# Kernel optimization log

Measured on AMD Instinct MI355X. Metric: run time of the kernel, lower is better.

## Reference

```python
import jax, jax.numpy as jnp
import numpy as np

B, N, F_IN = 1, 4096, 128
H, F_OUT = 8, 64
NEG = -1e9


def setup_inputs() -> dict:
    key = jax.random.key(0)
    ks = jax.random.split(key, 7)
    x = jax.random.normal(ks[0], (B, N, F_IN), dtype=jnp.float32)
    edge = jax.random.uniform(ks[1], (N, N)) < 0.02
    edge = edge | jnp.eye(N, dtype=bool)
    adj = jnp.where(edge, 0.0, NEG).astype(jnp.float32)
    # Glorot-uniform params
    def glorot(k, shape, fan_in, fan_out):
        lim = float(np.sqrt(6.0 / (fan_in + fan_out)))
        return jax.random.uniform(k, shape, jnp.float32, -lim, lim)
    W_proj = glorot(ks[2], (H * F_OUT, F_IN), F_IN, H * F_OUT)      # linear_proj.weight
    a_src = glorot(ks[3], (1, H, F_OUT), H, F_OUT)                   # scoring_fn_source
    a_tgt = glorot(ks[4], (1, H, F_OUT), H, F_OUT)                   # scoring_fn_target
    W_skip = glorot(ks[5], (H * F_OUT, F_IN), F_IN, H * F_OUT)       # skip_proj.weight
    bias = jnp.zeros((H * F_OUT,), dtype=jnp.float32)
    return {"in_nodes_features": x, "adj": adj, "W_proj": W_proj,
            "a_src": a_src, "a_tgt": a_tgt, "W_skip": W_skip, "bias": bias}


def reference(in_nodes_features, adj, W_proj, a_src, a_tgt, W_skip, bias):
    x = in_nodes_features                                  # [B,N,Fin]  (dropout p=0)
    proj = jnp.einsum('bnf,of->bno', x, W_proj)            # [B,N,H*Fo]
    proj = proj.reshape(B, N, H, F_OUT)                    # [B,N,H,Fo]
    s_src = jnp.einsum('bnhd,xhd->bhn', proj, a_src)       # [B,H,N] (row / source)
    s_tgt = jnp.einsum('bnhd,xhd->bhn', proj, a_tgt)       # [B,H,N] (col / target)
    scores = s_src[:, :, :, None] + s_tgt[:, :, None, :]   # [B,H,N,N]
    scores = jax.nn.leaky_relu(scores, negative_slope=0.2)
    att = jax.nn.softmax(scores + adj, axis=-1)            # adj additive mask, broadcast over B,H
    out = jnp.einsum('bhij,bjhd->bihd', att, proj)         # [B,N,H,Fo]
    out = out + jnp.einsum('bnf,of->bno', x, W_skip).reshape(B, N, H, F_OUT)  # skip (dims differ)
    out = out.reshape(B, N, H * F_OUT) + bias              # concat + bias
    out = jax.nn.elu(out)                                  # activation ELU
    return out, adj
```

## Files before the change

### kernel.cpp

```cpp
#include <hip/hip_runtime.h>
#include <cmath>

#define N_NODES 4096
#define FIN     128
#define H_HEADS 8
#define FOUT    64
#define HF      512
#define CAP     256

typedef float  vf4 __attribute__((ext_vector_type(4)));
typedef float  vf2 __attribute__((ext_vector_type(2)));
typedef unsigned int vu4 __attribute__((ext_vector_type(4)));

__device__ __forceinline__ unsigned short f2bf(float f) {
    unsigned u = __float_as_uint(f);
    u += 0x7fff + ((u >> 16) & 1);
    return (unsigned short)(u >> 16);
}

__global__ __launch_bounds__(256) void gemm_fused(
    const float* __restrict__ x, const float* __restrict__ Wp,
    const float* __restrict__ Ws, const float* __restrict__ a_src,
    const float* __restrict__ a_tgt,
    unsigned short* __restrict__ proj, float* __restrict__ skip,
    float* __restrict__ ssrc, float* __restrict__ stgt)
{
    __shared__ __align__(16) float AsT[64][68];
    __shared__ __align__(16) float BsT[64][68];

    const int t  = threadIdx.x;
    const int rb = blockIdx.y * 64;
    const int cb = blockIdx.x * 64;
    const bool isP = (cb < HF);
    const float* Wbase = isP ? (Wp + cb * FIN) : (Ws + (cb - HF) * FIN);

    const int tx = t & 15;
    const int ty = t >> 4;
    float acc[4][4] = {{0.f}};

    for (int kb = 0; kb < FIN; kb += 64) {
        #pragma unroll
        for (int p = 0; p < 4; ++p) {
            int f4 = t + p * 256;
            int r  = f4 >> 4;
            int k4 = f4 & 15;
            float4 a = *(const float4*)(x + (size_t)(rb + r) * FIN + kb + k4 * 4);
            AsT[k4*4+0][r] = a.x; AsT[k4*4+1][r] = a.y;
            AsT[k4*4+2][r] = a.z; AsT[k4*4+3][r] = a.w;
            float4 b = *(const float4*)(Wbase + (size_t)r * FIN + kb + k4 * 4);
            BsT[k4*4+0][r] = b.x; BsT[k4*4+1][r] = b.y;
            BsT[k4*4+2][r] = b.z; BsT[k4*4+3][r] = b.w;
        }
        __syncthreads();
        #pragma unroll 8
        for (int kk = 0; kk < 64; ++kk) {
            float4 a = *(const float4*)&AsT[kk][ty * 4];
            float4 b = *(const float4*)&BsT[kk][tx * 4];
            acc[0][0] += a.x*b.x; acc[0][1] += a.x*b.y; acc[0][2] += a.x*b.z; acc[0][3] += a.x*b.w;
            acc[1][0] += a.y*b.x; acc[1][1] += a.y*b.y; acc[1][2] += a.y*b.z; acc[1][3] += a.y*b.w;
            acc[2][0] += a.z*b.x; acc[2][1] += a.z*b.y; acc[2][2] += a.z*b.z; acc[2][3] += a.z*b.w;
            acc[3][0] += a.w*b.x; acc[3][1] += a.w*b.y; acc[3][2] += a.w*b.z; acc[3][3] += a.w*b.w;
        }
        __syncthreads();
    }

    if (isP) {
        #pragma unroll
        for (int i = 0; i < 4; ++i) {
            ushort4 v;
            v.x = f2bf(acc[i][0]); v.y = f2bf(acc[i][1]);
            v.z = f2bf(acc[i][2]); v.w = f2bf(acc[i][3]);
            *(ushort4*)(proj + (size_t)(rb + ty*4 + i) * HF + cb + tx * 4) = v;
        }
        const int h = cb >> 6;
        const float as0 = a_src[cb + tx*4 + 0], as1 = a_src[cb + tx*4 + 1];
        const float as2 = a_src[cb + tx*4 + 2], as3 = a_src[cb + tx*4 + 3];
        const float at0 = a_tgt[cb + tx*4 + 0], at1 = a_tgt[cb + tx*4 + 1];
        const float at2 = a_tgt[cb + tx*4 + 2], at3 = a_tgt[cb + tx*4 + 3];
        #pragma unroll
        for (int i = 0; i < 4; ++i) {
            float ps = acc[i][0]*as0 + acc[i][1]*as1 + acc[i][2]*as2 + acc[i][3]*as3;
            float pt = acc[i][0]*at0 + acc[i][1]*at1 + acc[i][2]*at2 + acc[i][3]*at3;
            #pragma unroll
            for (int off = 1; off < 16; off <<= 1) {
                ps += __shfl_xor(ps, off);
                pt += __shfl_xor(pt, off);
            }
            if (tx == 0) {
                int n = rb + ty*4 + i;
                ssrc[n * H_HEADS + h] = ps;
                stgt[n * H_HEADS + h] = pt;
            }
        }
    } else {
        #pragma unroll
        for (int i = 0; i < 4; ++i) {
            float4 v = make_float4(acc[i][0], acc[i][1], acc[i][2], acc[i][3]);
            *(float4*)(skip + (size_t)(rb + ty*4 + i) * HF + (cb - HF) + tx * 4) = v;
        }
    }
}

__global__ __launch_bounds__(512) void att_kernel(
    const float* __restrict__ adj, const unsigned short* __restrict__ proj,
    const float* __restrict__ skip, const float* __restrict__ ssrc,
    const float* __restrict__ stgt, const float* __restrict__ bias,
    float* __restrict__ out, float* __restrict__ adj_out)
{
    __shared__ int   s_idx[CAP];
    __shared__ float sp[H_HEADS][CAP];
    __shared__ float s_i[H_HEADS];
    __shared__ int   s_cnt;

    const int t    = threadIdx.x;
    const int i    = blockIdx.x;
    const int lane = t & 63;
    if (t == 0) s_cnt = 0;
    if (t < H_HEADS) s_i[t] = ssrc[i * H_HEADS + t];
    __syncthreads();

    const vf4* arow = (const vf4*)(adj + (size_t)i * N_NODES);
    vf4 va[2];
    const unsigned long long lt = (1ull << lane) - 1ull;
    #pragma unroll
    for (int it = 0; it < 2; ++it) {
        const int f4 = t + it * 512;
        vf4 v = __builtin_nontemporal_load(arow + f4);
        va[it] = v;
        const int jb = (f4 * 4) << 10;
        const bool h0 = (v.x == 0.f), h1 = (v.y == 0.f), h2 = (v.z == 0.f), h3 = (v.w == 0.f);
        const unsigned long long b0 = __ballot(h0), b1 = __ballot(h1);
        const unsigned long long b2 = __ballot(h2), b3 = __ballot(h3);
        const int n0 = __popcll(b0), n1 = __popcll(b1), n2 = __popcll(b2);
        const int total = n0 + n1 + n2 + __popcll(b3);
        int base = 0;
        if (lane == 0 && total) base = atomicAdd(&s_cnt, total);
        base = __shfl(base, 0);
        if (h0) { int p = base + __popcll(b0 & lt);                if (p < CAP) s_idx[p] = jb;        }
        if (h1) { int p = base + n0 + __popcll(b1 & lt);           if (p < CAP) s_idx[p] = jb + 1024; }
        if (h2) { int p = base + n0 + n1 + __popcll(b2 & lt);      if (p < CAP) s_idx[p] = jb + 2048; }
        if (h3) { int p = base + n0 + n1 + n2 + __popcll(b3 & lt); if (p < CAP) s_idx[p] = jb + 3072; }
    }
    __syncthreads();
    const int c = (s_cnt < CAP) ? s_cnt : CAP;

    for (int k = t; k < c; k += 512) {
        const float* st = (const float*)((const char*)stgt + (s_idx[k] >> 5));
        float4 t0 = *(const float4*)(st);
        float4 t1 = *(const float4*)(st + 4);
        float e;
        e = s_i[0] + t0.x; sp[0][k] = (e > 0.f) ? e : 0.2f * e;
        e = s_i[1] + t0.y; sp[1][k] = (e > 0.f) ? e : 0.2f * e;
        e = s_i[2] + t0.z; sp[2][k] = (e > 0.f) ? e : 0.2f * e;
        e = s_i[3] + t0.w; sp[3][k] = (e > 0.f) ? e : 0.2f * e;
        e = s_i[4] + t1.x; sp[4][k] = (e > 0.f) ? e : 0.2f * e;
        e = s_i[5] + t1.y; sp[5][k] = (e > 0.f) ? e : 0.2f * e;
        e = s_i[6] + t1.z; sp[6][k] = (e > 0.f) ? e : 0.2f * e;
        e = s_i[7] + t1.w; sp[7][k] = (e > 0.f) ? e : 0.2f * e;
    }
    __syncthreads();

    const int h = t >> 6;
    float m = -1e30f;
    for (int k = lane; k < c; k += 64) m = fmaxf(m, sp[h][k]);
    #pragma unroll
    for (int off = 32; off; off >>= 1) m = fmaxf(m, __shfl_xor(m, off));
    float l = 0.0f;
    for (int k = lane; k < c; k += 64) {
        float e = __expf(sp[h][k] - m);
        sp[h][k] = e;
        l += e;
    }
    #pragma unroll
    for (int off = 32; off; off >>= 1) l += __shfl_xor(l, off);
    const float inv = 1.0f / l;

    const int g  = lane >> 3;
    const int k8 = lane & 7;
    vf2 a2[4] = {{0.f, 0.f}, {0.f, 0.f}, {0.f, 0.f}, {0.f, 0.f}};
    const char* pbase = (const char*)proj + h * FOUT * 2 + k8 * 16;
    #pragma unroll 2
    for (int k = g; k < c; k += 8) {
        const int   off = s_idx[k];
        const float p   = sp[h][k];
        const vf2   p2  = {p, p};
        vu4 raw = *(const vu4*)(pbase + off);
        vf2 v0 = { __uint_as_float(raw.x << 16), __uint_as_float(raw.x & 0xffff0000u) };
        vf2 v1 = { __uint_as_float(raw.y << 16), __uint_as_float(raw.y & 0xffff0000u) };
        vf2 v2 = { __uint_as_float(raw.z << 16), __uint_as_float(raw.z & 0xffff0000u) };
        vf2 v3 = { __uint_as_float(raw.w << 16), __uint_as_float(raw.w & 0xffff0000u) };
        a2[0] += p2 * v0; a2[1] += p2 * v1; a2[2] += p2 * v2; a2[3] += p2 * v3;
    }
    float a8[8] = {a2[0].x, a2[0].y, a2[1].x, a2[1].y,
                   a2[2].x, a2[2].y, a2[3].x, a2[3].y};
    #pragma unroll
    for (int off = 8; off < 64; off <<= 1) {
        #pragma unroll
        for (int q = 0; q < 8; ++q) a8[q] += __shfl_xor(a8[q], off);
    }
    if (g == 0) {
        const int o = h * FOUT + k8 * 8;
        const float* sk = skip + (size_t)i * HF + o;
        const float* bs = bias + o;
        float r[8];
        #pragma unroll
        for (int q = 0; q < 8; ++q) {
            float v = a8[q] * inv + sk[q] + bs[q];
            r[q] = (v > 0.f) ? v : expm1f(v);
        }
        *(float4*)(out + (size_t)i * HF + o)     = make_float4(r[0], r[1], r[2], r[3]);
        *(float4*)(out + (size_t)i * HF + o + 4) = make_float4(r[4], r[5], r[6], r[7]);
    }

    vf4* aout = (vf4*)(adj_out + (size_t)i * N_NODES);
    __builtin_nontemporal_store(va[0], aout + t);
    __builtin_nontemporal_store(va[1], aout + t + 512);
}

extern "C" void kernel_launch(void* const* d_in, const int* in_sizes, int n_in,
                              void* d_out, int out_size, void* d_ws, size_t ws_size,
                              hipStream_t stream)
{
    const float* x     = (const float*)d_in[0];
    const float* adj   = (const float*)d_in[1];
    const float* Wp    = (const float*)d_in[2];
    const float* a_src = (const float*)d_in[3];
    const float* a_tgt = (const float*)d_in[4];
    const float* Ws    = (const float*)d_in[5];
    const float* bias  = (const float*)d_in[6];

    float* out     = (float*)d_out;
    float* adj_out = out + (size_t)N_NODES * HF;

    unsigned short* proj = (unsigned short*)d_ws;
    float* ssrc = (float*)((char*)d_ws + (size_t)N_NODES * HF * sizeof(unsigned short));
    float* stgt = ssrc + (size_t)N_NODES * H_HEADS;
    float* skip = out;

    gemm_fused<<<dim3(16, 64), 256, 0, stream>>>(x, Wp, Ws, a_src, a_tgt,
                                                 proj, skip, ssrc, stgt);
    att_kernel<<<N_NODES, 512, 0, stream>>>(adj, proj, skip, ssrc, stgt, bias,
                                            out, adj_out);
}
```

Before: 191.8 us.

## Overlap adjacency scan and copy with projection GEMM in one fused launch

The adjacency row scan (neighbor index compaction) and the adj_out copy move out of the attention kernel into extra blocks of the GEMM launch, so the memory-bound 64MB adj read/write can overlap the compute-bound projection GEMM. Neighbor indices and counts go to a global workspace, zeroed by a memset, and the attention kernel reads them back. The GEMM K-tile is halved to 32 to shrink shared memory and raise occupancy. The cost is an extra memset, a global round trip for the indices, and global atomics in place of shared-memory atomics.

```diff
diff --git a/kernel.cpp b/kernel.cpp
--- a/kernel.cpp
+++ b/kernel.cpp
@@ -7,6 +7,7 @@
 #define FOUT    64
 #define HF      512
 #define CAP     256
+#define GEMM_BLOCKS 1024
 
 typedef float  vf4 __attribute__((ext_vector_type(4)));
 typedef float  vf2 __attribute__((ext_vector_type(2)));
@@ -18,134 +19,142 @@
     return (unsigned short)(u >> 16);
 }
 
-__global__ __launch_bounds__(256) void gemm_fused(
+__global__ __launch_bounds__(256) void k1_fused(
     const float* __restrict__ x, const float* __restrict__ Wp,
     const float* __restrict__ Ws, const float* __restrict__ a_src,
-    const float* __restrict__ a_tgt,
+    const float* __restrict__ a_tgt, const float* __restrict__ adj,
     unsigned short* __restrict__ proj, float* __restrict__ skip,
-    float* __restrict__ ssrc, float* __restrict__ stgt)
+    float* __restrict__ ssrc, float* __restrict__ stgt,
+    int* __restrict__ cnt, int* __restrict__ idx,
+    float* __restrict__ adj_out)
 {
-    __shared__ __align__(16) float AsT[64][68];
-    __shared__ __align__(16) float BsT[64][68];
-
+    __shared__ __align__(16) float smem[2 * 32 * 68];
+    const int bx = blockIdx.x;
     const int t  = threadIdx.x;
-    const int rb = blockIdx.y * 64;
-    const int cb = blockIdx.x * 64;
-    const bool isP = (cb < HF);
-    const float* Wbase = isP ? (Wp + cb * FIN) : (Ws + (cb - HF) * FIN);
-
-    const int tx = t & 15;
-    const int ty = t >> 4;
-    float acc[4][4] = {{0.f}};
-
-    for (int kb = 0; kb < FIN; kb += 64) {
+
+    if (bx < GEMM_BLOCKS) {
+        float (*AsT)[68] = (float(*)[68])smem;
+        float (*BsT)[68] = (float(*)[68])(smem + 32 * 68);
+        const int rb = (bx >> 4) * 64;
+        const int cb = (bx & 15) * 64;
+        const bool isP = (cb < HF);
+        const float* Wbase = isP ? (Wp + cb * FIN) : (Ws + (cb - HF) * FIN);
+
+        const int tx = t & 15;
+        const int ty = t >> 4;
+        float acc[4][4] = {{0.f}};
+
+        for (int kb = 0; kb < FIN; kb += 32) {
+            #pragma unroll
+            for (int p = 0; p < 2; ++p) {
+                int f4 = t + p * 256;
+                int r  = f4 >> 3;
+                int k4 = f4 & 7;
+                float4 a = *(const float4*)(x + (size_t)(rb + r) * FIN + kb + k4 * 4);
+                AsT[k4*4+0][r] = a.x; AsT[k4*4+1][r] = a.y;
+                AsT[k4*4+2][r] = a.z; AsT[k4*4+3][r] = a.w;
+                float4 b = *(const float4*)(Wbase + (size_t)r * FIN + kb + k4 * 4);
+                BsT[k4*4+0][r] = b.x; BsT[k4*4+1][r] = b.y;
+                BsT[k4*4+2][r] = b.z; BsT[k4*4+3][r] = b.w;
+            }
+            __syncthreads();
+            #pragma unroll 8
+            for (int kk = 0; kk < 32; ++kk) {
+                float4 a = *(const float4*)&AsT[kk][ty * 4];
+                float4 b = *(const float4*)&BsT[kk][tx * 4];
+                acc[0][0] += a.x*b.x; acc[0][1] += a.x*b.y; acc[0][2] += a.x*b.z; acc[0][3] += a.x*b.w;
+                acc[1][0] += a.y*b.x; acc[1][1] += a.y*b.y; acc[1][2] += a.y*b.z; acc[1][3] += a.y*b.w;
+                acc[2][0] += a.z*b.x; acc[2][1] += a.z*b.y; acc[2][2] += a.z*b.z; acc[2][3] += a.z*b.w;
+                acc[3][0] += a.w*b.x; acc[3][1] += a.w*b.y; acc[3][2] += a.w*b.z; acc[3][3] += a.w*b.w;
+            }
+            __syncthreads();
+        }
+
+        if (isP) {
+            #pragma unroll
+            for (int i = 0; i < 4; ++i) {
+                ushort4 v;
+                v.x = f2bf(acc[i][0]); v.y = f2bf(acc[i][1]);
+                v.z = f2bf(acc[i][2]); v.w = f2bf(acc[i][3]);
+                *(ushort4*)(proj + (size_t)(rb + ty*4 + i) * HF + cb + tx * 4) = v;
+            }
+            const int h = cb >> 6;
+            const float as0 = a_src[cb + tx*4 + 0], as1 = a_src[cb + tx*4 + 1];
+            const float as2 = a_src[cb + tx*4 + 2], as3 = a_src[cb + tx*4 + 3];
+            const float at0 = a_tgt[cb + tx*4 + 0], at1 = a_tgt[cb + tx*4 + 1];
+            const float at2 = a_tgt[cb + tx*4 + 2], at3 = a_tgt[cb + tx*4 + 3];
+            #pragma unroll
+            for (int i = 0; i < 4; ++i) {
+                float ps = acc[i][0]*as0 + acc[i][1]*as1 + acc[i][2]*as2 + acc[i][3]*as3;
+                float pt = acc[i][0]*at0 + acc[i][1]*at1 + acc[i][2]*at2 + acc[i][3]*at3;
+                #pragma unroll
+                for (int off = 1; off < 16; off <<= 1) {
+                    ps += __shfl_xor(ps, off);
+                    pt += __shfl_xor(pt, off);
+                }
+                if (tx == 0) {
+                    int n = rb + ty*4 + i;
+                    ssrc[n * H_HEADS + h] = ps;
+                    stgt[n * H_HEADS + h] = pt;
+                }
+            }
+        } else {
+            #pragma unroll
+            for (int i = 0; i < 4; ++i) {
+                float4 v = make_float4(acc[i][0], acc[i][1], acc[i][2], acc[i][3]);
+                *(float4*)(skip + (size_t)(rb + ty*4 + i) * HF + (cb - HF) + tx * 4) = v;
+            }
+        }
+    } else {
+        const int i    = bx - GEMM_BLOCKS;
+        const int lane = t & 63;
+        const unsigned long long lt = (1ull << lane) - 1ull;
+        const vf4* arow = (const vf4*)(adj + (size_t)i * N_NODES);
+        vf4*       aout = (vf4*)(adj_out + (size_t)i * N_NODES);
+        int* rowidx = idx + i * CAP;
         #pragma unroll
-        for (int p = 0; p < 4; ++p) {
-            int f4 = t + p * 256;
-            int r  = f4 >> 4;
-            int k4 = f4 & 15;
-            float4 a = *(const float4*)(x + (size_t)(rb + r) * FIN + kb + k4 * 4);
-            AsT[k4*4+0][r] = a.x; AsT[k4*4+1][r] = a.y;
-            AsT[k4*4+2][r] = a.z; AsT[k4*4+3][r] = a.w;
-            float4 b = *(const float4*)(Wbase + (size_t)r * FIN + kb + k4 * 4);
-            BsT[k4*4+0][r] = b.x; BsT[k4*4+1][r] = b.y;
-            BsT[k4*4+2][r] = b.z; BsT[k4*4+3][r] = b.w;
-        }
-        __syncthreads();
-        #pragma unroll 8
-        for (int kk = 0; kk < 64; ++kk) {
-            float4 a = *(const float4*)&AsT[kk][ty * 4];
-            float4 b = *(const float4*)&BsT[kk][tx * 4];
-            acc[0][0] += a.x*b.x; acc[0][1] += a.x*b.y; acc[0][2] += a.x*b.z; acc[0][3] += a.x*b.w;
-            acc[1][0] += a.y*b.x; acc[1][1] += a.y*b.y; acc[1][2] += a.y*b.z; acc[1][3] += a.y*b.w;
-            acc[2][0] += a.z*b.x; acc[2][1] += a.z*b.y; acc[2][2] += a.z*b.z; acc[2][3] += a.z*b.w;
-            acc[3][0] += a.w*b.x; acc[3][1] += a.w*b.y; acc[3][2] += a.w*b.z; acc[3][3] += a.w*b.w;
-        }
-        __syncthreads();
-    }
-
-    if (isP) {
-        #pragma unroll
-        for (int i = 0; i < 4; ++i) {
-            ushort4 v;
-            v.x = f2bf(acc[i][0]); v.y = f2bf(acc[i][1]);
-            v.z = f2bf(acc[i][2]); v.w = f2bf(acc[i][3]);
-            *(ushort4*)(proj + (size_t)(rb + ty*4 + i) * HF + cb + tx * 4) = v;
-        }
-        const int h = cb >> 6;
-        const float as0 = a_src[cb + tx*4 + 0], as1 = a_src[cb + tx*4 + 1];
-        const float as2 = a_src[cb + tx*4 + 2], as3 = a_src[cb + tx*4 + 3];
-        const float at0 = a_tgt[cb + tx*4 + 0], at1 = a_tgt[cb + tx*4 + 1];
-        const float at2 = a_tgt[cb + tx*4 + 2], at3 = a_tgt[cb + tx*4 + 3];
-        #pragma unroll
-        for (int i = 0; i < 4; ++i) {
-            float ps = acc[i][0]*as0 + acc[i][1]*as1 + acc[i][2]*as2 + acc[i][3]*as3;
-            float pt = acc[i][0]*at0 + acc[i][1]*at1 + acc[i][2]*at2 + acc[i][3]*at3;
-            #pragma unroll
-            for (int off = 1; off < 16; off <<= 1) {
-                ps += __shfl_xor(ps, off);
-                pt += __shfl_xor(pt, off);
-            }
-            if (tx == 0) {
-                int n = rb + ty*4 + i;
-                ssrc[n * H_HEADS + h] = ps;
-                stgt[n * H_HEADS + h] = pt;
-            }
-        }
-    } else {
-        #pragma unroll
-        for (int i = 0; i < 4; ++i) {
-            float4 v = make_float4(acc[i][0], acc[i][1], acc[i][2], acc[i][3]);
-            *(float4*)(skip + (size_t)(rb + ty*4 + i) * HF + (cb - HF) + tx * 4) = v;
+        for (int it = 0; it < 4; ++it) {
+            const int f4 = t + it * 256;
+            vf4 v = __builtin_nontemporal_load(arow + f4);
+            __builtin_nontemporal_store(v, aout + f4);
+            const int jb = (f4 * 4) << 10;
+            const bool h0 = (v.x == 0.f), h1 = (v.y == 0.f), h2 = (v.z == 0.f), h3 = (v.w == 0.f);
+            const unsigned long long b0 = __ballot(h0), b1 = __ballot(h1);
+            const unsigned long long b2 = __ballot(h2), b3 = __ballot(h3);
+            const int n0 = __popcll(b0), n1 = __popcll(b1), n2 = __popcll(b2);
+            const int total = n0 + n1 + n2 + __popcll(b3);
+            int base = 0;
+            if (lane == 0 && total) base = atomicAdd(&cnt[i], total);
+            base = __shfl(base, 0);
+            if (h0) { int p = base + __popcll(b0 & lt);                if (p < CAP) rowidx[p] = jb;        }
+            if (h1) { int p = base + n0 + __popcll(b1 & lt);           if (p < CAP) rowidx[p] = jb + 1024; }
+            if (h2) { int p = base + n0 + n1 + __popcll(b2 & lt);      if (p < CAP) rowidx[p] = jb + 2048; }
+            if (h3) { int p = base + n0 + n1 + n2 + __popcll(b3 & lt); if (p < CAP) rowidx[p] = jb + 3072; }
         }
     }
 }
 
 __global__ __launch_bounds__(512) void att_kernel(
-    const float* __restrict__ adj, const unsigned short* __restrict__ proj,
-    const float* __restrict__ skip, const float* __restrict__ ssrc,
-    const float* __restrict__ stgt, const float* __restrict__ bias,
-    float* __restrict__ out, float* __restrict__ adj_out)
+    const unsigned short* __restrict__ proj, const float* __restrict__ skip,
+    const float* __restrict__ ssrc, const float* __restrict__ stgt,
+    const float* __restrict__ bias, const int* __restrict__ cnt,
+    const int* __restrict__ idx, float* __restrict__ out)
 {
     __shared__ int   s_idx[CAP];
     __shared__ float sp[H_HEADS][CAP];
     __shared__ float s_i[H_HEADS];
-    __shared__ int   s_cnt;
 
     const int t    = threadIdx.x;
     const int i    = blockIdx.x;
     const int lane = t & 63;
-    if (t == 0) s_cnt = 0;
     if (t < H_HEADS) s_i[t] = ssrc[i * H_HEADS + t];
+    int c = cnt[i]; if (c > CAP) c = CAP;
     __syncthreads();
 
-    const vf4* arow = (const vf4*)(adj + (size_t)i * N_NODES);
-    vf4 va[2];
-    const unsigned long long lt = (1ull << lane) - 1ull;
-    #pragma unroll
-    for (int it = 0; it < 2; ++it) {
-        const int f4 = t + it * 512;
-        vf4 v = __builtin_nontemporal_load(arow + f4);
-        va[it] = v;
-        const int jb = (f4 * 4) << 10;
-        const bool h0 = (v.x == 0.f), h1 = (v.y == 0.f), h2 = (v.z == 0.f), h3 = (v.w == 0.f);
-        const unsigned long long b0 = __ballot(h0), b1 = __ballot(h1);
-        const unsigned long long b2 = __ballot(h2), b3 = __ballot(h3);
-        const int n0 = __popcll(b0), n1 = __popcll(b1), n2 = __popcll(b2);
-        const int total = n0 + n1 + n2 + __popcll(b3);
-        int base = 0;
-        if (lane == 0 && total) base = atomicAdd(&s_cnt, total);
-        base = __shfl(base, 0);
-        if (h0) { int p = base + __popcll(b0 & lt);                if (p < CAP) s_idx[p] = jb;        }
-        if (h1) { int p = base + n0 + __popcll(b1 & lt);           if (p < CAP) s_idx[p] = jb + 1024; }
-        if (h2) { int p = base + n0 + n1 + __popcll(b2 & lt);      if (p < CAP) s_idx[p] = jb + 2048; }
-        if (h3) { int p = base + n0 + n1 + n2 + __popcll(b3 & lt); if (p < CAP) s_idx[p] = jb + 3072; }
-    }
-    __syncthreads();
-    const int c = (s_cnt < CAP) ? s_cnt : CAP;
-
     for (int k = t; k < c; k += 512) {
-        const float* st = (const float*)((const char*)stgt + (s_idx[k] >> 5));
+        const int off = idx[i * CAP + k];
+        s_idx[k] = off;
+        const float* st = (const float*)((const char*)stgt + (off >> 5));
         float4 t0 = *(const float4*)(st);
         float4 t1 = *(const float4*)(st + 4);
         float e;
@@ -211,10 +220,6 @@
         *(float4*)(out + (size_t)i * HF + o)     = make_float4(r[0], r[1], r[2], r[3]);
         *(float4*)(out + (size_t)i * HF + o + 4) = make_float4(r[4], r[5], r[6], r[7]);
     }
-
-    vf4* aout = (vf4*)(adj_out + (size_t)i * N_NODES);
-    __builtin_nontemporal_store(va[0], aout + t);
-    __builtin_nontemporal_store(va[1], aout + t + 512);
 }
 
 extern "C" void kernel_launch(void* const* d_in, const int* in_sizes, int n_in,
@@ -233,12 +238,15 @@
     float* adj_out = out + (size_t)N_NODES * HF;
 
     unsigned short* proj = (unsigned short*)d_ws;
-    float* ssrc = (float*)((char*)d_ws + (size_t)N_NODES * HF * sizeof(unsigned short));
+    float* ssrc = (float*)((char*)d_ws + (size_t)N_NODES * HF * 2);
     float* stgt = ssrc + (size_t)N_NODES * H_HEADS;
+    int*   cnt  = (int*)(stgt + (size_t)N_NODES * H_HEADS);
+    int*   idxb = cnt + N_NODES;
     float* skip = out;
 
-    gemm_fused<<<dim3(16, 64), 256, 0, stream>>>(x, Wp, Ws, a_src, a_tgt,
-                                                 proj, skip, ssrc, stgt);
-    att_kernel<<<N_NODES, 512, 0, stream>>>(adj, proj, skip, ssrc, stgt, bias,
-                                            out, adj_out);
-}
+    hipMemsetAsync(cnt, 0, N_NODES * sizeof(int), stream);
+    k1_fused<<<GEMM_BLOCKS + N_NODES, 256, 0, stream>>>(
+        x, Wp, Ws, a_src, a_tgt, adj, proj, skip, ssrc, stgt, cnt, idxb, adj_out);
+    att_kernel<<<N_NODES, 512, 0, stream>>>(proj, skip, ssrc, stgt, bias,
+                                            cnt, idxb, out);
+}
```

After: 192.3 us. No clear change (+0.2%).
